# Kernel optimization log

Hardware: AMD Instinct MI355X
Metric: run time of the kernel (lower is better)

The kernel has to match this reference:

```python
import jax, jax.numpy as jnp
import numpy as np
from functools import partial

B, F, H, G, S = 8192, 16, 128, 4, 20  # batch, features, hidden, goals, SUBSTEPS
A_IZH, B_IZH, C_IZH, D_IZH = 0.02, 0.2, -65.0, 8.0  # Izhikevich 'RS' params
RATE_DECAY = 0.9
GAMMA, LR = 0.95, 1e-3


def izh_step(v, u, rate, I):
    """One Izhikevich substep (dt=1): returns new (v, u, rate, spike)."""
    v_new = v + (0.04 * v * v + 5.0 * v + 140.0 - u + I)
    u_new = u + A_IZH * (B_IZH * v - u)
    spike = (v_new >= 30.0).astype(v.dtype)
    v_new = jnp.where(spike > 0, C_IZH, v_new)
    u_new = u_new + spike * D_IZH
    rate_new = RATE_DECAY * rate + (1.0 - RATE_DECAY) * spike
    return v_new, u_new, rate_new, spike


def build_features(energy, threat, food_visible, goal, cls_probs, DA_, NA_):
    # [B,16] = [4 scalars | one-hot goal (4) | cls_probs (5) | DA | NA | hunger]
    base = jnp.stack([energy / 100.0, threat, food_visible, 1.0 - energy / 100.0], axis=-1)
    onehot = jax.nn.one_hot(goal, G, dtype=base.dtype)
    tail = jnp.stack([DA_, NA_, jnp.maximum(0.0, 0.5 - energy / 100.0)], axis=-1)
    return jnp.concatenate([base, onehot, cls_probs, tail], axis=-1)


def setup_inputs() -> dict:
    key = jax.random.key(0)
    ks = jax.random.split(key, 16)
    energy = jax.random.uniform(ks[0], (B,)) * 100.0
    threat = jax.random.uniform(ks[1], (B,))
    food_visible = jax.random.uniform(ks[2], (B,))
    goal = jax.random.randint(ks[3], (B,), 0, G)
    prev_goal = jax.random.randint(ks[4], (B,), 0, G)
    DA_ = jax.random.uniform(ks[5], (B,))
    NA_ = jax.random.uniform(ks[6], (B,))
    reward = jax.random.normal(ks[7], (B,)) * 0.5
    cls_probs = jax.nn.softmax(jax.random.normal(ks[8], (B, 5)), axis=-1)
    a_in = 0.5 * np.sqrt(6.0 / (F + H))   # xavier_uniform gain 0.5
    a_out = 0.3 * np.sqrt(6.0 / (H + G))  # xavier_uniform gain 0.3
    W_in_w = jax.random.uniform(ks[9], (B, H, F), minval=-a_in, maxval=a_in)
    W_in_b = jax.random.uniform(ks[10], (B, H), minval=-1.0, maxval=1.0) / np.sqrt(F)
    W_out_w = jax.random.uniform(ks[11], (B, G, H), minval=-a_out, maxval=a_out)
    W_out_b = jax.random.uniform(ks[12], (B, G), minval=-1.0, maxval=1.0) / np.sqrt(H)
    hv = jnp.full((B, H), -65.0)
    hu = B_IZH * hv
    hrate = jnp.zeros((B, H))
    vv = jnp.full((B, G), -65.0)
    vu = B_IZH * vv
    vrate = jnp.zeros((B, G))
    elig_in = jnp.zeros((B, H, F))
    elig_out = jnp.zeros((B, G, H))
    prev_values = jnp.zeros((B, G))
    prev_features = jax.random.uniform(ks[13], (B, F))
    noise = jax.random.normal(ks[14], (S, B, H))
    return dict(energy=energy, threat=threat, food_visible=food_visible, goal=goal,
                prev_goal=prev_goal, DA_=DA_, NA_=NA_, reward=reward, cls_probs=cls_probs,
                W_in_w=W_in_w, W_in_b=W_in_b, W_out_w=W_out_w, W_out_b=W_out_b,
                hv=hv, hu=hu, hrate=hrate, vv=vv, vu=vu, vrate=vrate,
                elig_in=elig_in, elig_out=elig_out, prev_values=prev_values,
                prev_features=prev_features, noise=noise)


def reference(energy, threat, food_visible, goal, prev_goal, DA_, NA_, reward, cls_probs,
              W_in_w, W_in_b, W_out_w, W_out_b, hv, hu, hrate, vv, vu, vrate,
              elig_in, elig_out, prev_values, prev_features, noise):
    features = build_features(energy, threat, food_visible, goal, cls_probs, DA_, NA_)  # [B,F]
    I_in = jnp.einsum('bhf,bf->bh', W_in_w, features) + W_in_b
    I_in = I_in * (5.0 / (jnp.mean(jnp.abs(I_in), axis=-1, keepdims=True) + 1e-8))

    def step(carry, nz):
        hv, hu, hrate, vv, vu, vrate, hsp, vsp = carry
        hv, hu, hrate, sp_h = izh_step(hv, hu, hrate, I_in + 0.3 * nz)
        I_out = jnp.einsum('bgh,bh->bg', W_out_w, hrate) + W_out_b
        I_out = I_out * (4.0 / (jnp.mean(jnp.abs(I_out), axis=-1, keepdims=True) + 1e-8))
        vv, vu, vrate, sp_v = izh_step(vv, vu, vrate, I_out)
        return (hv, hu, hrate, vv, vu, vrate, hsp + sp_h, vsp + sp_v), None

    carry0 = (hv, hu, hrate, vv, vu, vrate, jnp.zeros_like(hrate), jnp.zeros_like(vrate))
    (hv, hu, hrate, vv, vu, vrate, h_spikes, v_spikes), _ = jax.lax.scan(step, carry0, noise)

    values = jnp.einsum('bgh,bh->bg', W_out_w, hrate) + W_out_b  # [B,G]
    V_now = jnp.take_along_axis(values, goal[:, None], axis=1)[:, 0]
    V_prev = jnp.take_along_axis(prev_values, prev_goal[:, None], axis=1)[:, 0]
    td = reward + GAMMA * V_now - V_prev  # [B]

    elig_in_new = 0.9 * elig_in + hrate[:, :, None] * prev_features[:, None, :]
    elig_out_new = 0.9 * elig_out + vrate[:, :, None] * hrate[:, None, :]

    upd = (jnp.abs(td) > 1e-3)  # [B]
    scale = (LR * td * DA_)[:, None, None]
    W_in_new = jnp.where(upd[:, None, None], jnp.clip(W_in_w + scale * elig_in_new, -3.0, 3.0), W_in_w)
    W_out_new = jnp.where(upd[:, None, None], jnp.clip(W_out_w + scale * elig_out_new, -3.0, 3.0), W_out_w)

    hidden_active = jnp.mean((h_spikes > 0).astype(values.dtype), axis=-1)  # [B]
    return values, td, hidden_active, W_in_new, W_out_new, elig_in_new, elig_out_new
```

## Files before the change

kernel.cpp:

```cpp
#include <hip/hip_runtime.h>


namespace {

constexpr int F = 16;
constexpr int H = 128;
constexpr int G = 4;
constexpr int S = 20;
constexpr int HP = H + 1;

__device__ __forceinline__ float clip3(float x) {
    return fminf(fmaxf(x, -3.0f), 3.0f);
}

__global__ __launch_bounds__(128)
void spiking_critic_kernel(
    const float* __restrict__ energy,
    const float* __restrict__ threat,
    const float* __restrict__ food_visible,
    const int*   __restrict__ goal,
    const int*   __restrict__ prev_goal,
    const float* __restrict__ DA,
    const float* __restrict__ NA,
    const float* __restrict__ reward,
    const float* __restrict__ cls_probs,
    const float* __restrict__ W_in_w,
    const float* __restrict__ W_in_b,
    const float* __restrict__ W_out_w,
    const float* __restrict__ W_out_b,
    const float* __restrict__ hv_in,
    const float* __restrict__ hu_in,
    const float* __restrict__ hrate_in,
    const float* __restrict__ vv_in,
    const float* __restrict__ vu_in,
    const float* __restrict__ vrate_in,
    const float* __restrict__ elig_in,
    const float* __restrict__ elig_out,
    const float* __restrict__ prev_values,
    const float* __restrict__ prev_features,
    const float* __restrict__ noise,
    float* __restrict__ out_values,
    float* __restrict__ out_td,
    float* __restrict__ out_hidden,
    float* __restrict__ out_Win,
    float* __restrict__ out_Wout,
    float* __restrict__ out_ein,
    float* __restrict__ out_eout,
    int nB)
{
    const int b = blockIdx.x;
    const int t = threadIdx.x;

    __shared__ float w_out_lds[G * H];
    __shared__ float hrate_all[S * HP];
    __shared__ float hrfin_lds[H];
    __shared__ float feat[F];
    __shared__ float pf_lds[F];
    __shared__ float iout_all[S * G];
    __shared__ float wob[G];
    __shared__ float vrate_lds[G];
    __shared__ float red[2];
    __shared__ float tdsh;

    ((float4*)w_out_lds)[t] = ((const float4*)(W_out_w + (size_t)b * (G * H)))[t];
    if (t < F) pf_lds[t] = prev_features[(size_t)b * F + t];
    if (t < G) wob[t]    = W_out_b[(size_t)b * G + t];

    if (t < F) {
        float e = energy[b];
        float v;
        if      (t == 0)  v = e / 100.0f;
        else if (t == 1)  v = threat[b];
        else if (t == 2)  v = food_visible[b];
        else if (t == 3)  v = 1.0f - e / 100.0f;
        else if (t < 8)   v = (goal[b] == (t - 4)) ? 1.0f : 0.0f;
        else if (t < 13)  v = cls_probs[(size_t)b * 5 + (t - 8)];
        else if (t == 13) v = DA[b];
        else if (t == 14) v = NA[b];
        else              v = fmaxf(0.0f, 0.5f - e / 100.0f);
        feat[t] = v;
    }
    __syncthreads();

    const float4* wrow = (const float4*)(W_in_w + ((size_t)b * H + t) * F);
    float dot = 0.0f;
    #pragma unroll
    for (int j = 0; j < 4; ++j) {
        float4 w = wrow[j];
        dot += w.x * feat[4 * j + 0] + w.y * feat[4 * j + 1]
             + w.z * feat[4 * j + 2] + w.w * feat[4 * j + 3];
    }
    float Iraw = dot + W_in_b[(size_t)b * H + t];
    float a = fabsf(Iraw);
    #pragma unroll
    for (int m = 32; m >= 1; m >>= 1) a += __shfl_xor(a, m, 64);
    if ((t & 63) == 0) red[t >> 6] = a;
    __syncthreads();
    const float meanI = (red[0] + red[1]) * (1.0f / 128.0f);
    const float Iin = Iraw * (5.0f / (meanI + 1e-8f));

    float hv = hv_in[(size_t)b * H + t];
    float hu = hu_in[(size_t)b * H + t];
    float hr = hrate_in[(size_t)b * H + t];

    float nz[S];
    #pragma unroll
    for (int s = 0; s < S; ++s)
        nz[s] = noise[((size_t)s * nB + b) * H + t];

    float hsp = 0.0f;
    #pragma unroll
    for (int s = 0; s < S; ++s) {
        float I  = Iin + 0.3f * nz[s];
        float vn = hv + (0.04f * hv * hv + 5.0f * hv + 140.0f - hu + I);
        float un = hu + 0.02f * (0.2f * hv - hu);
        float sp = (vn >= 30.0f) ? 1.0f : 0.0f;
        hv = (sp > 0.0f) ? -65.0f : vn;
        hu = un + sp * 8.0f;
        hr = 0.9f * hr + 0.1f * sp;
        hsp += sp;
        hrate_all[s * HP + t] = hr;
    }
    hrfin_lds[t] = hr;
    __syncthreads();

    if (t < S * G) {
        const int s = t >> 2;
        const int g = t & 3;
        const float* __restrict__ wr   = w_out_lds + g * H;
        const float* __restrict__ hrow = hrate_all + s * HP;
        float acc = 0.0f;
        #pragma unroll 8
        for (int i = 0; i < H; ++i) {
            int h = (i + t) & (H - 1);
            acc = fmaf(wr[h], hrow[h], acc);
        }
        iout_all[t] = acc + wob[g];
    }
    __syncthreads();

    if (t < G) {
        float vvv = vv_in[(size_t)b * G + t];
        float vuu = vu_in[(size_t)b * G + t];
        float vrr = vrate_in[(size_t)b * G + t];
        #pragma unroll
        for (int s = 0; s < S; ++s) {
            float i0 = iout_all[4 * s + 0];
            float i1 = iout_all[4 * s + 1];
            float i2 = iout_all[4 * s + 2];
            float i3 = iout_all[4 * s + 3];
            float m4 = 0.25f * (fabsf(i0) + fabsf(i1) + fabsf(i2) + fabsf(i3));
            float Io = iout_all[4 * s + t] * (4.0f / (m4 + 1e-8f));
            float vn = vvv + (0.04f * vvv * vvv + 5.0f * vvv + 140.0f - vuu + Io);
            float un = vuu + 0.02f * (0.2f * vvv - vuu);
            float sp = (vn >= 30.0f) ? 1.0f : 0.0f;
            vvv = (sp > 0.0f) ? -65.0f : vn;
            vuu = un + sp * 8.0f;
            vrr = 0.9f * vrr + 0.1f * sp;
        }
        vrate_lds[t] = vrr;
        out_values[(size_t)b * G + t] = iout_all[4 * (S - 1) + t];
    }

    unsigned long long mb = __ballot(hsp > 0.0f);
    if ((t & 63) == 0) red[t >> 6] = (float)__popcll(mb);
    __syncthreads();

    if (t == 0) {
        float Vnow  = iout_all[4 * (S - 1) + goal[b]];
        float Vprev = prev_values[(size_t)b * G + prev_goal[b]];
        float td = reward[b] + 0.95f * Vnow - Vprev;
        out_td[b]     = td;
        out_hidden[b] = (red[0] + red[1]) * (1.0f / 128.0f);
        tdsh = td;
    }
    __syncthreads();

    const float td    = tdsh;
    const float scale = 1e-3f * td * DA[b];
    const bool  upd   = fabsf(td) > 1e-3f;

    {
        const float4* ei4 = (const float4*)(elig_in + (size_t)b * (H * F));
        const float4* wi4 = (const float4*)(W_in_w  + (size_t)b * (H * F));
        float4* oW = (float4*)(out_Win + (size_t)b * (H * F));
        float4* oE = (float4*)(out_ein + (size_t)b * (H * F));
        const float4* pf4 = (const float4*)pf_lds;
        #pragma unroll
        for (int k = 0; k < 4; ++k) {
            int q = t + 128 * k;
            int h = q >> 2;
            int j = q & 3;
            float4 e  = ei4[q];
            float4 pf = pf4[j];
            float  hrv = hrfin_lds[h];
            float4 en;
            en.x = 0.9f * e.x + hrv * pf.x;
            en.y = 0.9f * e.y + hrv * pf.y;
            en.z = 0.9f * e.z + hrv * pf.z;
            en.w = 0.9f * e.w + hrv * pf.w;
            oE[q] = en;
            float4 w = wi4[q];
            float4 wn;
            if (upd) {
                wn.x = clip3(w.x + scale * en.x);
                wn.y = clip3(w.y + scale * en.y);
                wn.z = clip3(w.z + scale * en.z);
                wn.w = clip3(w.w + scale * en.w);
            } else {
                wn = w;
            }
            oW[q] = wn;
        }
    }

    {
        const float4* eo4 = (const float4*)(elig_out + (size_t)b * (G * H));
        float4* oW = (float4*)(out_Wout + (size_t)b * (G * H));
        float4* oE = (float4*)(out_eout + (size_t)b * (G * H));
        int q  = t;
        int gg = q >> 5;
        int h0 = (q & 31) * 4;
        float4 e  = eo4[q];
        float  vrv = vrate_lds[gg];
        float4 en;
        en.x = 0.9f * e.x + vrv * hrfin_lds[h0 + 0];
        en.y = 0.9f * e.y + vrv * hrfin_lds[h0 + 1];
        en.z = 0.9f * e.z + vrv * hrfin_lds[h0 + 2];
        en.w = 0.9f * e.w + vrv * hrfin_lds[h0 + 3];
        oE[q] = en;
        float4 w = ((const float4*)w_out_lds)[q];
        float4 wn;
        if (upd) {
            wn.x = clip3(w.x + scale * en.x);
            wn.y = clip3(w.y + scale * en.y);
            wn.z = clip3(w.z + scale * en.z);
            wn.w = clip3(w.w + scale * en.w);
        } else {
            wn = w;
        }
        oW[q] = wn;
    }
}

}

extern "C" void kernel_launch(void* const* d_in, const int* in_sizes, int n_in,
                              void* d_out, int out_size, void* d_ws, size_t ws_size,
                              hipStream_t stream) {
    const int nB = in_sizes[0];

    float* out        = (float*)d_out;
    float* out_values = out;
    float* out_td     = out_values + (size_t)nB * G;
    float* out_hidden = out_td + nB;
    float* out_Win    = out_hidden + nB;
    float* out_Wout   = out_Win + (size_t)nB * H * F;
    float* out_ein    = out_Wout + (size_t)nB * G * H;
    float* out_eout   = out_ein + (size_t)nB * H * F;

    spiking_critic_kernel<<<dim3(nB), dim3(128), 0, stream>>>(
        (const float*)d_in[0],  (const float*)d_in[1],  (const float*)d_in[2],
        (const int*)  d_in[3],  (const int*)  d_in[4],
        (const float*)d_in[5],  (const float*)d_in[6],  (const float*)d_in[7],
        (const float*)d_in[8],  (const float*)d_in[9],  (const float*)d_in[10],
        (const float*)d_in[11], (const float*)d_in[12], (const float*)d_in[13],
        (const float*)d_in[14], (const float*)d_in[15], (const float*)d_in[16],
        (const float*)d_in[17], (const float*)d_in[18], (const float*)d_in[19],
        (const float*)d_in[20], (const float*)d_in[21], (const float*)d_in[22],
        (const float*)d_in[23],
        out_values, out_td, out_hidden, out_Win, out_Wout, out_ein, out_eout,
        nB);
}
```

Baseline: 393.7 us.

## Replace per-substep output GEMV with spike-mask sums and linear rate recurrence

```diff
diff --git a/kernel.cpp b/kernel.cpp
--- a/kernel.cpp
+++ b/kernel.cpp
@@ -52,19 +52,64 @@
     const int t = threadIdx.x;
 
     __shared__ float w_out_lds[G * H];
-    __shared__ float hrate_all[S * HP];
+    __shared__ float w_out_p[G * HP];
+    __shared__ float hr0_lds[H];
     __shared__ float hrfin_lds[H];
     __shared__ float feat[F];
     __shared__ float pf_lds[F];
-    __shared__ float iout_all[S * G];
+    __shared__ float Iin_lds[H];
+    __shared__ float C_lds[S * G];
+    __shared__ float Jpart[16];
+    __shared__ unsigned long long smask[2 * S];
     __shared__ float wob[G];
     __shared__ float vrate_lds[G];
     __shared__ float red[2];
+    __shared__ float red2[2];
     __shared__ float tdsh;
 
-    ((float4*)w_out_lds)[t] = ((const float4*)(W_out_w + (size_t)b * (G * H)))[t];
+    const float4* wi4 = (const float4*)(W_in_w + (size_t)b * (H * F));
+    float4 winq0 = wi4[t];
+    float4 winq1 = wi4[t + 128];
+    float4 winq2 = wi4[t + 256];
+    float4 winq3 = wi4[t + 384];
+    const float wib = W_in_b[(size_t)b * H + t];
+
+    float hv = hv_in[(size_t)b * H + t];
+    float hu = hu_in[(size_t)b * H + t];
+    float hr = hrate_in[(size_t)b * H + t];
+    hr0_lds[t] = hr;
+
+    float nz[S];
+    #pragma unroll
+    for (int s = 0; s < S; ++s)
+        nz[s] = noise[((size_t)s * nB + b) * H + t];
+
+    const float da = DA[b];
+
+    {
+        float4 wv = ((const float4*)(W_out_w + (size_t)b * (G * H)))[t];
+        ((float4*)w_out_lds)[t] = wv;
+        int g  = t >> 5;
+        int h0 = (t & 31) * 4;
+        float* wp = w_out_p + g * HP + h0;
+        wp[0] = wv.x; wp[1] = wv.y; wp[2] = wv.z; wp[3] = wv.w;
+    }
     if (t < F) pf_lds[t] = prev_features[(size_t)b * F + t];
     if (t < G) wob[t]    = W_out_b[(size_t)b * G + t];
+
+    float vvv = 0.0f, vuu = 0.0f, vrr = 0.0f;
+    int   gb  = 0;
+    float rw  = 0.0f, Vprev = 0.0f;
+    if (t < G) {
+        vvv = vv_in[(size_t)b * G + t];
+        vuu = vu_in[(size_t)b * G + t];
+        vrr = vrate_in[(size_t)b * G + t];
+        gb  = goal[b];
+    }
+    if (t == 0) {
+        rw    = reward[b];
+        Vprev = prev_values[(size_t)b * G + prev_goal[b]];
+    }
 
     if (t < F) {
         float e = energy[b];
@@ -75,22 +120,34 @@
         else if (t == 3)  v = 1.0f - e / 100.0f;
         else if (t < 8)   v = (goal[b] == (t - 4)) ? 1.0f : 0.0f;
         else if (t < 13)  v = cls_probs[(size_t)b * 5 + (t - 8)];
-        else if (t == 13) v = DA[b];
+        else if (t == 13) v = da;
         else if (t == 14) v = NA[b];
         else              v = fmaxf(0.0f, 0.5f - e / 100.0f);
         feat[t] = v;
     }
     __syncthreads();
 
-    const float4* wrow = (const float4*)(W_in_w + ((size_t)b * H + t) * F);
-    float dot = 0.0f;
-    #pragma unroll
-    for (int j = 0; j < 4; ++j) {
-        float4 w = wrow[j];
-        dot += w.x * feat[4 * j + 0] + w.y * feat[4 * j + 1]
-             + w.z * feat[4 * j + 2] + w.w * feat[4 * j + 3];
-    }
-    float Iraw = dot + W_in_b[(size_t)b * H + t];
+    {
+        const float4 fq = ((const float4*)feat)[t & 3];
+        float d0 = winq0.x * fq.x + winq0.y * fq.y + winq0.z * fq.z + winq0.w * fq.w;
+        float d1 = winq1.x * fq.x + winq1.y * fq.y + winq1.z * fq.z + winq1.w * fq.w;
+        float d2 = winq2.x * fq.x + winq2.y * fq.y + winq2.z * fq.z + winq2.w * fq.w;
+        float d3 = winq3.x * fq.x + winq3.y * fq.y + winq3.z * fq.z + winq3.w * fq.w;
+        d0 += __shfl_xor(d0, 1); d0 += __shfl_xor(d0, 2);
+        d1 += __shfl_xor(d1, 1); d1 += __shfl_xor(d1, 2);
+        d2 += __shfl_xor(d2, 1); d2 += __shfl_xor(d2, 2);
+        d3 += __shfl_xor(d3, 1); d3 += __shfl_xor(d3, 2);
+        if ((t & 3) == 0) {
+            int r = t >> 2;
+            Iin_lds[r]      = d0;
+            Iin_lds[r + 32] = d1;
+            Iin_lds[r + 64] = d2;
+            Iin_lds[r + 96] = d3;
+        }
+    }
+    __syncthreads();
+
+    float Iraw = Iin_lds[t] + wib;
     float a = fabsf(Iraw);
     #pragma unroll
     for (int m = 32; m >= 1; m >>= 1) a += __shfl_xor(a, m, 64);
@@ -98,15 +155,6 @@
     __syncthreads();
     const float meanI = (red[0] + red[1]) * (1.0f / 128.0f);
     const float Iin = Iraw * (5.0f / (meanI + 1e-8f));
-
-    float hv = hv_in[(size_t)b * H + t];
-    float hu = hu_in[(size_t)b * H + t];
-    float hr = hrate_in[(size_t)b * H + t];
-
-    float nz[S];
-    #pragma unroll
-    for (int s = 0; s < S; ++s)
-        nz[s] = noise[((size_t)s * nB + b) * H + t];
 
     float hsp = 0.0f;
     #pragma unroll
@@ -119,38 +167,64 @@
         hu = un + sp * 8.0f;
         hr = 0.9f * hr + 0.1f * sp;
         hsp += sp;
-        hrate_all[s * HP + t] = hr;
+        unsigned long long mb = __ballot(sp > 0.0f);
+        if ((t & 63) == 0) smask[2 * s + (t >> 6)] = mb;
     }
     hrfin_lds[t] = hr;
+    {
+        unsigned long long mb = __ballot(hsp > 0.0f);
+        if ((t & 63) == 0) red2[t >> 6] = (float)__popcll(mb);
+    }
     __syncthreads();
 
     if (t < S * G) {
         const int s = t >> 2;
         const int g = t & 3;
-        const float* __restrict__ wr   = w_out_lds + g * H;
-        const float* __restrict__ hrow = hrate_all + s * HP;
+        const float* __restrict__ wr = w_out_p + g * HP;
         float acc = 0.0f;
-        #pragma unroll 8
-        for (int i = 0; i < H; ++i) {
-            int h = (i + t) & (H - 1);
-            acc = fmaf(wr[h], hrow[h], acc);
-        }
-        iout_all[t] = acc + wob[g];
+        unsigned long long m0 = smask[2 * s];
+        unsigned long long m1 = smask[2 * s + 1];
+        while (m0) {
+            int h = __builtin_ctzll(m0);
+            m0 &= (m0 - 1);
+            acc += wr[h];
+        }
+        while (m1) {
+            int h = __builtin_ctzll(m1);
+            m1 &= (m1 - 1);
+            acc += wr[64 + h];
+        }
+        C_lds[t] = acc;
+    } else if (t < S * G + 16) {
+        const int u = t - S * G;
+        const int g = u & 3;
+        const int q = u >> 2;
+        const float* __restrict__ wr = w_out_p + g * HP + q * 32;
+        const float* __restrict__ h0 = hr0_lds + q * 32;
+        float a0 = 0.0f, a1 = 0.0f, a2 = 0.0f, a3 = 0.0f;
+        #pragma unroll
+        for (int i = 0; i < 32; i += 4) {
+            a0 = fmaf(wr[i + 0], h0[i + 0], a0);
+            a1 = fmaf(wr[i + 1], h0[i + 1], a1);
+            a2 = fmaf(wr[i + 2], h0[i + 2], a2);
+            a3 = fmaf(wr[i + 3], h0[i + 3], a3);
+        }
+        Jpart[u] = (a0 + a1) + (a2 + a3);
     }
     __syncthreads();
 
     if (t < G) {
-        float vvv = vv_in[(size_t)b * G + t];
-        float vuu = vu_in[(size_t)b * G + t];
-        float vrr = vrate_in[(size_t)b * G + t];
+        float J = (Jpart[t] + Jpart[t + 4]) + (Jpart[t + 8] + Jpart[t + 12]);
+        const float wb = wob[t];
         #pragma unroll
         for (int s = 0; s < S; ++s) {
-            float i0 = iout_all[4 * s + 0];
-            float i1 = iout_all[4 * s + 1];
-            float i2 = iout_all[4 * s + 2];
-            float i3 = iout_all[4 * s + 3];
-            float m4 = 0.25f * (fabsf(i0) + fabsf(i1) + fabsf(i2) + fabsf(i3));
-            float Io = iout_all[4 * s + t] * (4.0f / (m4 + 1e-8f));
+            J = 0.9f * J + 0.1f * C_lds[4 * s + t];
+            float Ir = J + wb;
+            float aa = fabsf(Ir);
+            aa += __shfl_xor(aa, 1);
+            aa += __shfl_xor(aa, 2);
+            float m4 = 0.25f * aa;
+            float Io = Ir * (4.0f / (m4 + 1e-8f));
             float vn = vvv + (0.04f * vvv * vvv + 5.0f * vvv + 140.0f - vuu + Io);
             float un = vuu + 0.02f * (0.2f * vvv - vuu);
             float sp = (vn >= 30.0f) ? 1.0f : 0.0f;
@@ -159,40 +233,34 @@
             vrr = 0.9f * vrr + 0.1f * sp;
         }
         vrate_lds[t] = vrr;
-        out_values[(size_t)b * G + t] = iout_all[4 * (S - 1) + t];
-    }
-
-    unsigned long long mb = __ballot(hsp > 0.0f);
-    if ((t & 63) == 0) red[t >> 6] = (float)__popcll(mb);
-    __syncthreads();
-
-    if (t == 0) {
-        float Vnow  = iout_all[4 * (S - 1) + goal[b]];
-        float Vprev = prev_values[(size_t)b * G + prev_goal[b]];
-        float td = reward[b] + 0.95f * Vnow - Vprev;
-        out_td[b]     = td;
-        out_hidden[b] = (red[0] + red[1]) * (1.0f / 128.0f);
-        tdsh = td;
+        float val = J + wb;
+        out_values[(size_t)b * G + t] = val;
+        float vg = __shfl(val, gb, 4);
+        if (t == 0) {
+            float td = rw + 0.95f * vg - Vprev;
+            out_td[b]     = td;
+            out_hidden[b] = (red2[0] + red2[1]) * (1.0f / 128.0f);
+            tdsh = td;
+        }
     }
     __syncthreads();
 
     const float td    = tdsh;
-    const float scale = 1e-3f * td * DA[b];
+    const float scale = 1e-3f * td * da;
     const bool  upd   = fabsf(td) > 1e-3f;
 
     {
         const float4* ei4 = (const float4*)(elig_in + (size_t)b * (H * F));
-        const float4* wi4 = (const float4*)(W_in_w  + (size_t)b * (H * F));
         float4* oW = (float4*)(out_Win + (size_t)b * (H * F));
         float4* oE = (float4*)(out_ein + (size_t)b * (H * F));
         const float4* pf4 = (const float4*)pf_lds;
+        const float4 pf = pf4[t & 3];
+        float4 wq[4] = {winq0, winq1, winq2, winq3};
         #pragma unroll
         for (int k = 0; k < 4; ++k) {
             int q = t + 128 * k;
             int h = q >> 2;
-            int j = q & 3;
             float4 e  = ei4[q];
-            float4 pf = pf4[j];
             float  hrv = hrfin_lds[h];
             float4 en;
             en.x = 0.9f * e.x + hrv * pf.x;
@@ -200,7 +268,7 @@
             en.z = 0.9f * e.z + hrv * pf.z;
             en.w = 0.9f * e.w + hrv * pf.w;
             oE[q] = en;
-            float4 w = wi4[q];
+            float4 w = wq[k];
             float4 wn;
             if (upd) {
                 wn.x = clip3(w.x + scale * en.x);
```

New measurement: 397.9 us. No clear change (+1.0%).
